# Kernel tuning notes

Measured on AMD Instinct MI355X. Metric: run time of the kernel, lower is better.

Reference implementation:

```python
import jax, jax.numpy as jnp
import numpy as np

TEMPERATURE = 0.2
LAMBDA_GAMMA = 0.5
LAMBDA_REG = 1e-4
LAMBDA_MARGIN = 0.8
NUM_USERS = 100000
NUM_ITEMS = 50000
EMBED_DIM = 64
BATCH = 8192


def setup_inputs() -> dict:
    key = jax.random.key(0)
    k1, k2, k3, k4, k5 = jax.random.split(key, 5)
    # Xavier-uniform-like scale for embedding tables
    bound = float(np.sqrt(6.0 / (NUM_USERS + EMBED_DIM)))
    user_table = jax.random.uniform(k1, (NUM_USERS, EMBED_DIM), jnp.float32, -bound, bound)
    bound_i = float(np.sqrt(6.0 / (NUM_ITEMS + EMBED_DIM)))
    item_table = jax.random.uniform(k2, (NUM_ITEMS, EMBED_DIM), jnp.float32, -bound_i, bound_i)
    user = jax.random.randint(k3, (BATCH,), 0, NUM_USERS, dtype=jnp.int64 if jax.config.jax_enable_x64 else jnp.int32)
    positive = jax.random.randint(k4, (BATCH,), 0, NUM_ITEMS, dtype=user.dtype)
    negative = jax.random.randint(k5, (BATCH,), 0, NUM_ITEMS, dtype=user.dtype)
    return {"user_table": user_table, "item_table": item_table,
            "user": user, "positive": positive, "negative": negative}


def _l2_normalize(x, eps=1e-12):
    # matches torch.nn.functional.normalize(dim=1)
    n = jnp.linalg.norm(x, axis=1, keepdims=True)
    return x / jnp.maximum(n, eps)


def _cscf_loss(e1, e2, temperature, margin):
    e1 = _l2_normalize(e1)  # [B, D]
    e2 = _l2_normalize(e2)  # [B, D]
    sim = jnp.sum(e1 * e2, axis=-1)  # [B]
    pos_score = jnp.exp(sim / temperature) + jnp.exp(jax.nn.relu(sim - margin) / temperature)
    # [B, B] score matrix: cross similarities plus self similarities
    total = jnp.matmul(e1, e2.T) + jnp.matmul(e1, e1.T)
    total = jnp.exp(total / temperature) + jnp.exp(jax.nn.relu(total - margin) / temperature)
    total = jnp.sum(total, axis=1)  # [B]
    loss = -jnp.log(pos_score / total + 1e-5)
    return jnp.mean(loss)


def _bpr_loss(u, p, n):
    pos = jnp.sum(u * p, axis=-1)
    neg = jnp.sum(u * n, axis=-1)
    return -jnp.mean(jax.nn.log_sigmoid(pos - neg))


def _reg_loss(u, p, n):
    b = u.shape[0]
    return 0.5 * (jnp.sum(u ** 2) + jnp.sum(p ** 2) + jnp.sum(n ** 2)) / b


def reference(user_table, item_table, user, positive, negative):
    ue = user_table[user]      # [B, D]
    pe = item_table[positive]  # [B, D]
    ne = item_table[negative]  # [B, D]
    bpr = _bpr_loss(ue, pe, ne)
    reg = LAMBDA_REG * _reg_loss(ue, pe, ne)
    na = LAMBDA_GAMMA * _cscf_loss(ue, pe, TEMPERATURE, LAMBDA_MARGIN)
    return (bpr, reg, na)
```

## Files before the change

kernel.cpp:

```cpp
#include <hip/hip_runtime.h>
#include <hip/hip_bf16.h>

#define BATCH 8192
#define DIM 64
#define TINV 5.0f
#define MARGIN 0.8f
#define CGT 1.01831563889f
#define LGAMMA 0.5f
#define LREG 1e-4f

typedef __attribute__((ext_vector_type(8))) short short8;
typedef __attribute__((ext_vector_type(4))) float float4v;

__device__ __forceinline__ unsigned short f2bf(float f) {
    unsigned int u = __builtin_bit_cast(unsigned int, f);
    unsigned int r = (u + 0x7fffu + ((u >> 16) & 1u)) >> 16;
    return (unsigned short)r;
}

__global__ __launch_bounds__(256) void phase1(
    const float* __restrict__ utab,
    const float* __restrict__ itab,
    const int* __restrict__ user, const int* __restrict__ posi,
    const int* __restrict__ negi,
    unsigned short* __restrict__ e1_out, unsigned short* __restrict__ g_out,
    float* __restrict__ pos_score, float* __restrict__ row_bpr,
    float* __restrict__ row_reg)
{
    const int lane = threadIdx.x & 63;
    const int wid = blockIdx.x * 4 + (threadIdx.x >> 6);

    for (int r = wid; r < BATCH; r += 1024) {
        const int ui = user[r], pi = posi[r], ni = negi[r];
        const float u = utab[(size_t)ui * DIM + lane];
        const float p = itab[(size_t)pi * DIM + lane];
        const float n = itab[(size_t)ni * DIM + lane];
        float up = u * p, un = u * n, uu = u * u, pp = p * p, nn = n * n;
        #pragma unroll
        for (int off = 32; off; off >>= 1) {
            up += __shfl_xor(up, off);
            un += __shfl_xor(un, off);
            uu += __shfl_xor(uu, off);
            pp += __shfl_xor(pp, off);
            nn += __shfl_xor(nn, off);
        }
        const float nu = fmaxf(sqrtf(uu), 1e-12f);
        const float npn = fmaxf(sqrtf(pp), 1e-12f);
        const float e1 = u / nu;
        const float e2 = p / npn;
        e1_out[r * DIM + lane] = f2bf(e1);
        g_out[r * DIM + lane]  = f2bf(e1 + e2);
        if (lane == 0) {
            const float sim = up / (nu * npn);
            pos_score[r] = __expf(sim * TINV) + __expf(fmaxf(sim - MARGIN, 0.0f) * TINV);
            const float x = up - un;
            const float ax = fabsf(x);
            row_bpr[r] = fmaxf(-x, 0.0f) + logf(1.0f + __expf(-ax));
            row_reg[r] = uu + pp + nn;
        }
    }
}

__global__ __launch_bounds__(256) void phase2(
    const unsigned short* __restrict__ e1,
    const unsigned short* __restrict__ g,
    float* __restrict__ total)
{
    const int w = threadIdx.x >> 6;
    const int lane = threadIdx.x & 63;
    const int r0 = blockIdx.x * 64;
    const int jslice = blockIdx.y;
    const int rowsel = lane & 15;
    const int kbase = (lane >> 4) * 8;

    short8 a[4][2];
    #pragma unroll
    for (int rt = 0; rt < 4; rt++)
        #pragma unroll
        for (int ks = 0; ks < 2; ks++)
            a[rt][ks] = *(const short8*)&e1[(r0 + rt * 16 + rowsel) * DIM + ks * 32 + kbase];

    float rowacc[4][4];
    #pragma unroll
    for (int rt = 0; rt < 4; rt++)
        #pragma unroll
        for (int q = 0; q < 4; q++) rowacc[rt][q] = 0.0f;

    for (int it = 0; it < 8; it++) {
        const int j0 = jslice * 2048 + it * 256 + w * 64;
        short8 b[4][2];
        #pragma unroll
        for (int ct = 0; ct < 4; ct++)
            #pragma unroll
            for (int ks = 0; ks < 2; ks++)
                b[ct][ks] = *(const short8*)&g[(j0 + ct * 16 + rowsel) * DIM + ks * 32 + kbase];

        #pragma unroll
        for (int rt = 0; rt < 4; rt++) {
            #pragma unroll
            for (int ct = 0; ct < 4; ct++) {
                float4v acc = {0.0f, 0.0f, 0.0f, 0.0f};
                acc = __builtin_amdgcn_mfma_f32_16x16x32_bf16(a[rt][0], b[ct][0], acc, 0, 0, 0);
                acc = __builtin_amdgcn_mfma_f32_16x16x32_bf16(a[rt][1], b[ct][1], acc, 0, 0, 0);
                #pragma unroll
                for (int q = 0; q < 4; q++) {
                    const float s = acc[q];
                    const float e = __expf(s * TINV);
                    const float c = (s > MARGIN) ? CGT : 1.0f;
                    const float d = (s > MARGIN) ? 0.0f : 1.0f;
                    rowacc[rt][q] += fmaf(e, c, d);
                }
            }
        }
    }

    #pragma unroll
    for (int off = 1; off < 16; off <<= 1)
        #pragma unroll
        for (int rt = 0; rt < 4; rt++)
            #pragma unroll
            for (int q = 0; q < 4; q++)
                rowacc[rt][q] += __shfl_xor(rowacc[rt][q], off);

    if ((lane & 15) == 0) {
        const int rquad = lane >> 4;
        #pragma unroll
        for (int rt = 0; rt < 4; rt++)
            #pragma unroll
            for (int q = 0; q < 4; q++)
                atomicAdd(&total[r0 + rt * 16 + rquad * 4 + q], rowacc[rt][q]);
    }
}

__global__ __launch_bounds__(256) void phase3(
    const float* __restrict__ pos_score, const float* __restrict__ total,
    const float* __restrict__ row_bpr, const float* __restrict__ row_reg,
    float* __restrict__ out)
{
    __shared__ float rb[256], rr[256], rn[256];
    float sb = 0.0f, sr = 0.0f, sn = 0.0f;
    for (int i = threadIdx.x; i < BATCH; i += 256) {
        sb += row_bpr[i];
        sr += row_reg[i];
        sn += -__logf(pos_score[i] / total[i] + 1e-5f);
    }
    rb[threadIdx.x] = sb; rr[threadIdx.x] = sr; rn[threadIdx.x] = sn;
    __syncthreads();
    for (int off = 128; off; off >>= 1) {
        if (threadIdx.x < off) {
            rb[threadIdx.x] += rb[threadIdx.x + off];
            rr[threadIdx.x] += rr[threadIdx.x + off];
            rn[threadIdx.x] += rn[threadIdx.x + off];
        }
        __syncthreads();
    }
    if (threadIdx.x == 0) {
        out[0] = rb[0] / (float)BATCH;
        out[1] = LREG * 0.5f * rr[0] / (float)BATCH;
        out[2] = LGAMMA * (rn[0] / (float)BATCH);
    }
}

extern "C" void kernel_launch(void* const* d_in, const int* in_sizes, int n_in,
                              void* d_out, int out_size, void* d_ws, size_t ws_size,
                              hipStream_t stream) {
    const float* utab = (const float*)d_in[0];
    const float* itab = (const float*)d_in[1];
    const int* user = (const int*)d_in[2];
    const int* posi = (const int*)d_in[3];
    const int* negi = (const int*)d_in[4];

    char* ws = (char*)d_ws;
    unsigned short* e1 = (unsigned short*)ws;
    unsigned short* g  = (unsigned short*)(ws + (size_t)BATCH * DIM * 2);
    float* pos_score = (float*)(ws + 2 * (size_t)BATCH * DIM * 2);
    float* total     = pos_score + BATCH;
    float* row_bpr   = total + BATCH;
    float* row_reg   = row_bpr + BATCH;

    hipMemsetAsync(total, 0, BATCH * sizeof(float), stream);

    phase1<<<256, 256, 0, stream>>>(utab, itab, user, posi, negi,
                                    e1, g, pos_score, row_bpr, row_reg);
    phase2<<<dim3(128, 4), 256, 0, stream>>>(e1, g, total);
    phase3<<<1, 256, 0, stream>>>(pos_score, total, row_bpr, row_reg,
                                  (float*)d_out);
}
```

Measured before the change: 127.2 us.

## Prescale e1 for exp2, fuse memset, vectorize gather, widen phase2 grid

Phase1 now handles four rows per wave using float4 loads, and it zeroes the total buffer itself so the separate memset launch goes away. e1 is stored prescaled by 5/ln2, so phase2 can call exp2f directly and write the margin term as max(e*exp(-4),1) in place of compares and selects. Phase2 is split into twice as many j-slices to raise occupancy, at the cost of more atomics. Phase3 switches to 1024 threads with a wave-shuffle reduction. Prescaling before the bf16 rounding shifts precision slightly, and the code relies on the whole grid zeroing total before phase2 runs.

```diff
diff --git a/kernel.cpp b/kernel.cpp
--- a/kernel.cpp
+++ b/kernel.cpp
@@ -5,7 +5,8 @@
 #define DIM 64
 #define TINV 5.0f
 #define MARGIN 0.8f
-#define CGT 1.01831563889f
+#define SCALE5 7.21347520444f
+#define EM4 0.01831563889f
 #define LGAMMA 0.5f
 #define LREG 1e-4f
 
@@ -25,39 +26,55 @@
     const int* __restrict__ negi,
     unsigned short* __restrict__ e1_out, unsigned short* __restrict__ g_out,
     float* __restrict__ pos_score, float* __restrict__ row_bpr,
-    float* __restrict__ row_reg)
+    float* __restrict__ row_reg, float* __restrict__ total)
 {
+    const int tid  = blockIdx.x * 256 + threadIdx.x;
+    if (tid < BATCH) total[tid] = 0.0f;
+
     const int lane = threadIdx.x & 63;
-    const int wid = blockIdx.x * 4 + (threadIdx.x >> 6);
-
-    for (int r = wid; r < BATCH; r += 1024) {
-        const int ui = user[r], pi = posi[r], ni = negi[r];
-        const float u = utab[(size_t)ui * DIM + lane];
-        const float p = itab[(size_t)pi * DIM + lane];
-        const float n = itab[(size_t)ni * DIM + lane];
-        float up = u * p, un = u * n, uu = u * u, pp = p * p, nn = n * n;
-        #pragma unroll
-        for (int off = 32; off; off >>= 1) {
-            up += __shfl_xor(up, off);
-            un += __shfl_xor(un, off);
-            uu += __shfl_xor(uu, off);
-            pp += __shfl_xor(pp, off);
-            nn += __shfl_xor(nn, off);
-        }
-        const float nu = fmaxf(sqrtf(uu), 1e-12f);
-        const float npn = fmaxf(sqrtf(pp), 1e-12f);
-        const float e1 = u / nu;
-        const float e2 = p / npn;
-        e1_out[r * DIM + lane] = f2bf(e1);
-        g_out[r * DIM + lane]  = f2bf(e1 + e2);
-        if (lane == 0) {
-            const float sim = up / (nu * npn);
-            pos_score[r] = __expf(sim * TINV) + __expf(fmaxf(sim - MARGIN, 0.0f) * TINV);
-            const float x = up - un;
-            const float ax = fabsf(x);
-            row_bpr[r] = fmaxf(-x, 0.0f) + logf(1.0f + __expf(-ax));
-            row_reg[r] = uu + pp + nn;
-        }
+    const int wv   = tid >> 6;
+    const int sub  = lane >> 4;
+    const int l16  = lane & 15;
+    const int r    = wv * 4 + sub;
+
+    const int ui = user[r], pi = posi[r], ni = negi[r];
+    const float4 u = *(const float4*)&utab[(size_t)ui * DIM + l16 * 4];
+    const float4 p = *(const float4*)&itab[(size_t)pi * DIM + l16 * 4];
+    const float4 n = *(const float4*)&itab[(size_t)ni * DIM + l16 * 4];
+
+    float up = u.x*p.x + u.y*p.y + u.z*p.z + u.w*p.w;
+    float un = u.x*n.x + u.y*n.y + u.z*n.z + u.w*n.w;
+    float uu = u.x*u.x + u.y*u.y + u.z*u.z + u.w*u.w;
+    float pp = p.x*p.x + p.y*p.y + p.z*p.z + p.w*p.w;
+    float nn = n.x*n.x + n.y*n.y + n.z*n.z + n.w*n.w;
+    #pragma unroll
+    for (int off = 1; off < 16; off <<= 1) {
+        up += __shfl_xor(up, off);
+        un += __shfl_xor(un, off);
+        uu += __shfl_xor(uu, off);
+        pp += __shfl_xor(pp, off);
+        nn += __shfl_xor(nn, off);
+    }
+    const float nu  = fmaxf(sqrtf(uu), 1e-12f);
+    const float npn = fmaxf(sqrtf(pp), 1e-12f);
+    const float ia  = 1.0f / nu;
+    const float ib  = 1.0f / npn;
+    const float sa  = SCALE5 * ia;
+
+    union { unsigned short h[4]; uint2 v; } pe1, pg;
+    pe1.h[0] = f2bf(u.x * sa); pe1.h[1] = f2bf(u.y * sa);
+    pe1.h[2] = f2bf(u.z * sa); pe1.h[3] = f2bf(u.w * sa);
+    pg.h[0]  = f2bf(u.x * ia + p.x * ib); pg.h[1] = f2bf(u.y * ia + p.y * ib);
+    pg.h[2]  = f2bf(u.z * ia + p.z * ib); pg.h[3] = f2bf(u.w * ia + p.w * ib);
+    *(uint2*)&e1_out[r * DIM + l16 * 4] = pe1.v;
+    *(uint2*)&g_out[r * DIM + l16 * 4]  = pg.v;
+
+    if (l16 == 0) {
+        const float sim = up * (ia * ib);
+        pos_score[r] = __expf(sim * TINV) + __expf(fmaxf(sim - MARGIN, 0.0f) * TINV);
+        const float x = up - un;
+        row_bpr[r] = fmaxf(-x, 0.0f) + __logf(1.0f + __expf(-fabsf(x)));
+        row_reg[r] = uu + pp + nn;
     }
 }
 
@@ -86,8 +103,8 @@
         #pragma unroll
         for (int q = 0; q < 4; q++) rowacc[rt][q] = 0.0f;
 
-    for (int it = 0; it < 8; it++) {
-        const int j0 = jslice * 2048 + it * 256 + w * 64;
+    for (int it = 0; it < 4; it++) {
+        const int j0 = jslice * 1024 + it * 256 + w * 64;
         short8 b[4][2];
         #pragma unroll
         for (int ct = 0; ct < 4; ct++)
@@ -104,11 +121,8 @@
                 acc = __builtin_amdgcn_mfma_f32_16x16x32_bf16(a[rt][1], b[ct][1], acc, 0, 0, 0);
                 #pragma unroll
                 for (int q = 0; q < 4; q++) {
-                    const float s = acc[q];
-                    const float e = __expf(s * TINV);
-                    const float c = (s > MARGIN) ? CGT : 1.0f;
-                    const float d = (s > MARGIN) ? 0.0f : 1.0f;
-                    rowacc[rt][q] += fmaf(e, c, d);
+                    const float e = exp2f(acc[q]);
+                    rowacc[rt][q] += e + fmaxf(e * EM4, 1.0f);
                 }
             }
         }
@@ -132,32 +146,34 @@
     }
 }
 
-__global__ __launch_bounds__(256) void phase3(
+__global__ __launch_bounds__(1024) void phase3(
     const float* __restrict__ pos_score, const float* __restrict__ total,
     const float* __restrict__ row_bpr, const float* __restrict__ row_reg,
     float* __restrict__ out)
 {
-    __shared__ float rb[256], rr[256], rn[256];
+    __shared__ float rb[16], rr[16], rn[16];
     float sb = 0.0f, sr = 0.0f, sn = 0.0f;
-    for (int i = threadIdx.x; i < BATCH; i += 256) {
+    for (int i = threadIdx.x; i < BATCH; i += 1024) {
         sb += row_bpr[i];
         sr += row_reg[i];
         sn += -__logf(pos_score[i] / total[i] + 1e-5f);
     }
-    rb[threadIdx.x] = sb; rr[threadIdx.x] = sr; rn[threadIdx.x] = sn;
+    #pragma unroll
+    for (int off = 32; off; off >>= 1) {
+        sb += __shfl_xor(sb, off);
+        sr += __shfl_xor(sr, off);
+        sn += __shfl_xor(sn, off);
+    }
+    const int wid = threadIdx.x >> 6;
+    if ((threadIdx.x & 63) == 0) { rb[wid] = sb; rr[wid] = sr; rn[wid] = sn; }
     __syncthreads();
-    for (int off = 128; off; off >>= 1) {
-        if (threadIdx.x < off) {
-            rb[threadIdx.x] += rb[threadIdx.x + off];
-            rr[threadIdx.x] += rr[threadIdx.x + off];
-            rn[threadIdx.x] += rn[threadIdx.x + off];
-        }
-        __syncthreads();
-    }
     if (threadIdx.x == 0) {
-        out[0] = rb[0] / (float)BATCH;
-        out[1] = LREG * 0.5f * rr[0] / (float)BATCH;
-        out[2] = LGAMMA * (rn[0] / (float)BATCH);
+        float tb = 0.0f, tr = 0.0f, tn = 0.0f;
+        #pragma unroll
+        for (int i = 0; i < 16; i++) { tb += rb[i]; tr += rr[i]; tn += rn[i]; }
+        out[0] = tb / (float)BATCH;
+        out[1] = LREG * 0.5f * tr / (float)BATCH;
+        out[2] = LGAMMA * (tn / (float)BATCH);
     }
 }
 
@@ -178,11 +194,9 @@
     float* row_bpr   = total + BATCH;
     float* row_reg   = row_bpr + BATCH;
 
-    hipMemsetAsync(total, 0, BATCH * sizeof(float), stream);
-
-    phase1<<<256, 256, 0, stream>>>(utab, itab, user, posi, negi,
-                                    e1, g, pos_score, row_bpr, row_reg);
-    phase2<<<dim3(128, 4), 256, 0, stream>>>(e1, g, total);
-    phase3<<<1, 256, 0, stream>>>(pos_score, total, row_bpr, row_reg,
-                                  (float*)d_out);
-}
+    phase1<<<512, 256, 0, stream>>>(utab, itab, user, posi, negi,
+                                    e1, g, pos_score, row_bpr, row_reg, total);
+    phase2<<<dim3(128, 8), 256, 0, stream>>>(e1, g, total);
+    phase3<<<1, 1024, 0, stream>>>(pos_score, total, row_bpr, row_reg,
+                                   (float*)d_out);
+}
```

Result: faster. 114.5 us (-10.0%).
